# Kernel tuning notes

Measured on AMD Instinct MI355X. Metric: run time of the kernel, lower is better.

## Reference

```python
import jax, jax.numpy as jnp
import numpy as np

NEG = -1e30  # safe -inf surrogate for fp32 log-space DP
BLANK = 0


def setup_inputs() -> dict:
    key = jax.random.key(0)
    k1, k2 = jax.random.split(key)
    T, B, V, S = 2048, 64, 256, 256
    log_probs = jax.random.normal(k1, (T, B, V), dtype=jnp.float32)
    # targets exclude the blank index (0), as standard for CTC
    targets = jax.random.randint(k2, (B, S), 1, V).astype(jnp.int64)
    input_lengths = jnp.full((B,), T, dtype=jnp.int64)
    target_lengths = jnp.full((B,), S, dtype=jnp.int64)
    return {
        "log_probs": log_probs,
        "targets": targets,
        "input_lengths": input_lengths,
        "target_lengths": target_lengths,
    }


def _ctc_loss(log_probs, targets, input_lengths, target_lengths):
    """Numerically-stable CTC forward DP. log_probs: [T,B,V] (already log-softmaxed).
    Matches torch.nn.CTCLoss(blank=0, reduction='mean', zero_infinity=True)."""
    T, B, V = log_probs.shape
    S = targets.shape[1]
    L = 2 * S + 1  # extended label length (blanks interleaved)

    # extended label sequence: [blank, t0, blank, t1, ..., tS-1, blank]
    ext = jnp.full((B, L), BLANK, dtype=targets.dtype).at[:, 1::2].set(targets)

    # per-state emission log-probs: lp_ext[t, b, s] = log_probs[t, b, ext[b, s]]
    b_idx = jnp.arange(B)[:, None]
    lp_ext = log_probs[:, b_idx, ext]  # [T, B, L]

    # skip transition allowed when ext[s] != blank and ext[s] != ext[s-2]
    prev2 = jnp.pad(ext[:, :-2], ((0, 0), (2, 0)), constant_values=-1)
    skip = (ext != BLANK) & (ext != prev2)  # [B, L]

    alpha0 = jnp.full((B, L), NEG, dtype=log_probs.dtype)
    alpha0 = alpha0.at[:, 0].set(lp_ext[0, :, 0]).at[:, 1].set(lp_ext[0, :, 1])

    def step(alpha, xs):
        lp_t, t = xs
        a1 = jnp.pad(alpha[:, :-1], ((0, 0), (1, 0)), constant_values=NEG)
        a2 = jnp.pad(alpha[:, :-2], ((0, 0), (2, 0)), constant_values=NEG)
        comb = jnp.logaddexp(alpha, a1)
        comb = jnp.where(skip, jnp.logaddexp(comb, a2), comb)
        new = comb + lp_t
        # freeze alpha once past each sequence's input length
        new = jnp.where((t < input_lengths)[:, None], new, alpha)
        return new, None

    alpha, _ = jax.lax.scan(step, alpha0, (lp_ext[1:], jnp.arange(1, T)))

    end1 = jnp.take_along_axis(alpha, (2 * target_lengths)[:, None], axis=1)[:, 0]
    end2 = jnp.take_along_axis(alpha, (2 * target_lengths - 1)[:, None], axis=1)[:, 0]
    loss = -jnp.logaddexp(end1, end2)  # [B]

    # zero_infinity=True
    loss = jnp.where(jnp.isfinite(loss) & (loss < 1e29), loss, 0.0)
    # reduction='mean': divide each loss by its target length, then batch-mean
    return jnp.mean(loss / target_lengths.astype(loss.dtype))


def reference(log_probs, targets, input_lengths, target_lengths):
    # apply_log_softmax=True in the wrapper's forward
    log_probs = jax.nn.log_softmax(log_probs, axis=-1)
    return _ctc_loss(log_probs, targets, input_lengths, target_lengths)
```

## Files before the change

kernel.cpp:

```cpp
#include <hip/hip_runtime.h>
#include <hip/hip_fp16.h>
#include <stdint.h>

#define TT 2048
#define BB 64
#define VV 256
#define SS 256
#define LL 513

#define F_L2E 1.4426950408889634f
#define F_LN2 0.6931471805599453f
#define TGT_E 40
#define MARG  50
#define KOFF  262144

static __device__ __forceinline__ float exp2_fast(float x) {
  float r; asm("v_exp_f32 %0, %1" : "=v"(r) : "v"(x)); return r;
}
static __device__ __forceinline__ float log2_fast(float x) {
  float r; asm("v_log_f32 %0, %1" : "=v"(r) : "v"(x)); return r;
}
static __device__ __forceinline__ void g2l16(const void* g, void* l) {
  __builtin_amdgcn_global_load_lds((const __attribute__((address_space(1))) void*)g,
                                   (__attribute__((address_space(3))) void*)l, 16, 0, 0);
}
static __device__ __forceinline__ float dpp_shr1_f(float x) {
  int r = __builtin_amdgcn_update_dpp(0, __float_as_int(x), 0x138, 0xF, 0xF, true);
  return __int_as_float(r);
}
static __device__ __forceinline__ int dpp_shr1_i(int x) {
  return __builtin_amdgcn_update_dpp(0, x, 0x138, 0xF, 0xF, true);
}
template <int CTRL, int RMASK>
static __device__ __forceinline__ int dppmax_i(int v) {
  int d = __builtin_amdgcn_update_dpp(v, v, CTRL, RMASK, 0xF, false);
  return v > d ? v : d;
}
static __device__ __forceinline__ int scanmax_i(int v) {
  v = dppmax_i<0x111, 0xF>(v);
  v = dppmax_i<0x112, 0xF>(v);
  v = dppmax_i<0x114, 0xF>(v);
  v = dppmax_i<0x118, 0xF>(v);
  v = dppmax_i<0x142, 0xa>(v);
  v = dppmax_i<0x143, 0xc>(v);
  return v;
}

__global__ __launch_bounds__(256) void k_prep2(const float* __restrict__ lp,
                                               const int* __restrict__ tgt,
                                               __half* __restrict__ Eg,
                                               float* __restrict__ Bl,
                                               float* __restrict__ D2T) {
  __shared__ int tgtl[SS];
  __shared__ __half elds[4][VV];
  int b  = blockIdx.x & (BB - 1);
  int t0 = (blockIdx.x >> 6) << 2;
  int tid = threadIdx.x;
  tgtl[tid] = tgt[b * SS + tid];
  __syncthreads();
  int w = tid >> 6, lane = tid & 63;
  int t = t0 + w;
  float4 x = reinterpret_cast<const float4*>(lp + ((size_t)t * BB + b) * VV)[lane];
  float e0 = exp2_fast(x.x * F_L2E), e1 = exp2_fast(x.y * F_L2E);
  float e2 = exp2_fast(x.z * F_L2E), e3 = exp2_fast(x.w * F_L2E);
  float z = (e0 + e1) + (e2 + e3);
  z += __shfl_xor(z, 1);
  z += __shfl_xor(z, 2);
  z += __shfl_xor(z, 4);
  z += __shfl_xor(z, 8);
  z += __shfl_xor(z, 16);
  z += __shfl_xor(z, 32);
  elds[w][4 * lane + 0] = __float2half_rn(e0);
  elds[w][4 * lane + 1] = __float2half_rn(e1);
  elds[w][4 * lane + 2] = __float2half_rn(e2);
  elds[w][4 * lane + 3] = __float2half_rn(e3);
  asm volatile("s_waitcnt lgkmcnt(0)" ::: "memory");
  int s = 4 * lane;
  union { __half h[4]; uint2 u; } pk;
  pk.h[0] = elds[w][tgtl[s + 0]];
  pk.h[1] = elds[w][tgtl[s + 1]];
  pk.h[2] = elds[w][tgtl[s + 2]];
  pk.h[3] = elds[w][tgtl[s + 3]];
  reinterpret_cast<uint2*>(Eg + ((size_t)b * TT + t) * SS)[lane] = pk.u;
  if (lane == 0) {
    Bl[(size_t)b * TT + t]  = e0;
    D2T[(size_t)b * TT + t] = -log2_fast(z);
  }
}

__global__ __launch_bounds__(64) void k_ctc6(const __half* __restrict__ Eg,
                                             const float* __restrict__ Bl,
                                             const int* __restrict__ tgt,
                                             const int* __restrict__ ilen,
                                             const int* __restrict__ tlen,
                                             const float* __restrict__ D2T,
                                             float* __restrict__ lossw) {
  __shared__ float blanklds[TT];
  __shared__ float afin[LL];
  __shared__ int   cfinl[64];
  int b = blockIdx.x, lane = threadIdx.x;
  int len = ilen[b]; if (len > TT) len = TT; if (len < 0) len = 0;
  int tl  = tlen[b]; if (tl > SS) tl = SS; if (tl < 1) tl = 1;

  const float* blb = Bl  + (size_t)b * TT;
  const float* d2b = D2T + (size_t)b * TT;
  const uint2* eq  = reinterpret_cast<const uint2*>(Eg) + (size_t)b * TT * 64 + lane;

  int4 tv = reinterpret_cast<const int4*>(tgt + b * SS)[lane];
  int pw  = __shfl_up(tv.w, 1);
  float mk1 = (lane > 0 && tv.x != pw) ? 1.f : 0.f;
  float mk3 = (tv.y != tv.x) ? 1.f : 0.f;
  float mk5 = (tv.z != tv.y) ? 1.f : 0.f;
  float mk7 = (tv.w != tv.z) ? 1.f : 0.f;

#pragma unroll
  for (int j = 0; j < 8; ++j)
    g2l16(blb + j * 256 + lane * 4, &blanklds[j * 256]);

  uint2 pfA[16], pfB[16];
#pragma unroll
  for (int j = 0; j < 16; ++j) pfA[j] = eq[(size_t)j * 64];
  asm volatile("s_waitcnt vmcnt(0)" ::: "memory");

  float a0 = (lane == 0) ? 1.f : 0.f;
  float a1 = 0, a2 = 0, a3 = 0, a4 = 0, a5 = 0, a6 = 0, a7 = 0, a8 = 0;
  int C = 0;
  int diffi = 0;

#define STEP32(BANK, J, TB) do {                                               \
    uint2 pv = pf##BANK[J];                                                    \
    float2 flo = __half22float2(*reinterpret_cast<const __half2*>(&pv.x));     \
    float2 fhi = __half22float2(*reinterpret_cast<const __half2*>(&pv.y));     \
    float pb = blanklds[(TB) + (J)];                                           \
    float h1 = ldexpf(dpp_shr1_f(a7), diffi);                                  \
    a8 = (a8 + a7) * pb;                                                       \
    a7 = (a7 + a6 + mk7 * a5) * fhi.y;                                         \
    a6 = (a6 + a5) * pb;                                                       \
    a5 = (a5 + a4 + mk5 * a3) * fhi.x;                                         \
    a4 = (a4 + a3) * pb;                                                       \
    a3 = (a3 + a2 + mk3 * a1) * flo.y;                                         \
    a2 = (a2 + a1) * pb;                                                       \
    a1 = (a1 + a0 + mk1 * h1) * flo.x;                                         \
    a0 = (a0 + h1) * pb;                                                       \
  } while (0)

#define RESCALE8() do {                                                        \
    float mx = fmaxf(fmaxf(fmaxf(a0, a1), fmaxf(a2, a3)),                      \
                     fmaxf(fmaxf(a4, a5), fmaxf(fmaxf(a6, a7), a8)));          \
    bool live_ = (mx > 0.f);                                                   \
    int e_  = (int)((__float_as_uint(mx) >> 23) & 0xff);                       \
    int Cl_ = C + e_ - (127 + TGT_E);                                          \
    int key_ = live_ ? (Cl_ + KOFF) : 0;                                       \
    key_ = scanmax_i(key_);                                                    \
    int Cn_ = (key_ - KOFF) - MARG;                                            \
    if (live_ && Cl_ > Cn_) Cn_ = Cl_;                                         \
    int shE_ = Cn_ - C;                                                        \
    a0 = ldexpf(a0, -shE_); a1 = ldexpf(a1, -shE_); a2 = ldexpf(a2, -shE_);    \
    a3 = ldexpf(a3, -shE_); a4 = ldexpf(a4, -shE_); a5 = ldexpf(a5, -shE_);    \
    a6 = ldexpf(a6, -shE_); a7 = ldexpf(a7, -shE_); a8 = ldexpf(a8, -shE_);    \
    C = Cn_;                                                                   \
    diffi = dpp_shr1_i(C) - C;                                                 \
  } while (0)

#define ISSUE16(BANK, TBN) do {                                                \
    const uint2* p_ = eq + (size_t)(TBN) * 64;                                 \
    _Pragma("unroll")                                                          \
    for (int j_ = 0; j_ < 16; ++j_) pf##BANK[j_] = p_[(size_t)j_ * 64];        \
  } while (0)

#define BLK16(CUR, NXT, TB) do {                                               \
    int tbn_ = (TB) + 16; if (tbn_ > TT - 16) tbn_ = TT - 16;                  \
    ISSUE16(NXT, tbn_);                                                        \
    asm volatile("s_waitcnt vmcnt(16)" ::: "memory");                          \
    STEP32(CUR, 0, (TB));  STEP32(CUR, 1, (TB));  STEP32(CUR, 2, (TB));        \
    STEP32(CUR, 3, (TB));  STEP32(CUR, 4, (TB));  STEP32(CUR, 5, (TB));        \
    STEP32(CUR, 6, (TB));  STEP32(CUR, 7, (TB));                               \
    RESCALE8();                                                                \
    STEP32(CUR, 8, (TB));  STEP32(CUR, 9, (TB));  STEP32(CUR, 10, (TB));       \
    STEP32(CUR, 11, (TB)); STEP32(CUR, 12, (TB)); STEP32(CUR, 13, (TB));       \
    STEP32(CUR, 14, (TB)); STEP32(CUR, 15, (TB));                              \
    RESCALE8();                                                                \
  } while (0)

  int tcur = 0;
  for (int g = 0; g < TT / 32 && tcur + 32 <= len; ++g) {
    BLK16(A, B, tcur);
    BLK16(B, A, tcur + 16);
    tcur += 32;
  }

  if (tcur < len) {
    asm volatile("s_waitcnt vmcnt(0)" ::: "memory");
    while (tcur < len) {
      uint2 pv = eq[(size_t)tcur * 64];
      float2 flo = __half22float2(*reinterpret_cast<const __half2*>(&pv.x));
      float2 fhi = __half22float2(*reinterpret_cast<const __half2*>(&pv.y));
      float pb = blanklds[tcur];
      float h1 = ldexpf(dpp_shr1_f(a7), diffi);
      a8 = (a8 + a7) * pb;
      a7 = (a7 + a6 + mk7 * a5) * fhi.y;
      a6 = (a6 + a5) * pb;
      a5 = (a5 + a4 + mk5 * a3) * fhi.x;
      a4 = (a4 + a3) * pb;
      a3 = (a3 + a2 + mk3 * a1) * flo.y;
      a2 = (a2 + a1) * pb;
      a1 = (a1 + a0 + mk1 * h1) * flo.x;
      a0 = (a0 + h1) * pb;
      ++tcur;
      if ((tcur & 7) == 0) RESCALE8();
    }
  }

  float dsm = 0.f;
  for (int k2 = 0; k2 < TT / 64; ++k2) {
    int t2 = lane + 64 * k2;
    if (t2 < len) dsm += d2b[t2];
  }
  dsm += __shfl_xor(dsm, 1);
  dsm += __shfl_xor(dsm, 2);
  dsm += __shfl_xor(dsm, 4);
  dsm += __shfl_xor(dsm, 8);
  dsm += __shfl_xor(dsm, 16);
  dsm += __shfl_xor(dsm, 32);

  afin[8 * lane + 0] = a0; afin[8 * lane + 1] = a1;
  afin[8 * lane + 2] = a2; afin[8 * lane + 3] = a3;
  afin[8 * lane + 4] = a4; afin[8 * lane + 5] = a5;
  afin[8 * lane + 6] = a6; afin[8 * lane + 7] = a7;
  if (lane == 63) afin[512] = a8;
  cfinl[lane] = C;
  __syncthreads();
  if (lane == 0) {
    int s1 = 2 * tl, s2 = 2 * tl - 1;
    float v1 = afin[s1], v2 = afin[s2];
    int C1 = cfinl[s1 >= 512 ? 63 : (s1 >> 3)];
    int C2 = cfinl[s2 >= 512 ? 63 : (s2 >> 3)];
    float l1 = (v1 > 0.f) ? (log2_fast(v1) + (float)C1) : -1e30f;
    float l2 = (v2 > 0.f) ? (log2_fast(v2) + (float)C2) : -1e30f;
    float m  = fmaxf(l1, l2);
    float r  = m + log2_fast(exp2_fast(l1 - m) + exp2_fast(l2 - m));
    lossw[b] = -F_LN2 * (r + dsm);
  }
#undef STEP32
#undef RESCALE8
#undef ISSUE16
#undef BLK16
}

__global__ __launch_bounds__(64) void k_final(const float* __restrict__ lossw,
                                              const int* __restrict__ tlen,
                                              float* __restrict__ out) {
  int i = threadIdx.x;
  float v = lossw[i];
  float d = (float)tlen[i];
  v = (v < 1e29f && v > -1e30f) ? (v / d) : 0.f;
  v += __shfl_xor(v, 1);
  v += __shfl_xor(v, 2);
  v += __shfl_xor(v, 4);
  v += __shfl_xor(v, 8);
  v += __shfl_xor(v, 16);
  v += __shfl_xor(v, 32);
  if (i == 0) out[0] = v * (1.f / BB);
}

extern "C" void kernel_launch(void* const* d_in, const int* in_sizes, int n_in,
                              void* d_out, int out_size, void* d_ws, size_t ws_size,
                              hipStream_t stream) {
  const float* lp = (const float*)d_in[0];
  const int* tgt  = (const int*)d_in[1];
  const int* ilen = (const int*)d_in[2];
  const int* tlen = (const int*)d_in[3];

  size_t eg_bytes = (size_t)BB * TT * SS * 2;
  __half* Eg   = (__half*)d_ws;
  float* Bl    = (float*)((char*)d_ws + eg_bytes);
  float* D2T   = Bl + (size_t)BB * TT;
  float* lossw = D2T + (size_t)BB * TT;

  k_prep2<<<BB * (TT / 4), 256, 0, stream>>>(lp, tgt, Eg, Bl, D2T);
  k_ctc6<<<BB, 64, 0, stream>>>(Eg, Bl, tgt, ilen, tlen, D2T, lossw);
  k_final<<<1, 64, 0, stream>>>(lossw, tlen, (float*)d_out);
}
```

Before: 168.0 us.

## Triple-buffer emission prefetch and hoist blank-prob LDS reads in CTC recurrence

```diff
diff --git a/kernel.cpp b/kernel.cpp
--- a/kernel.cpp
+++ b/kernel.cpp
@@ -88,7 +88,7 @@
   }
 }
 
-__global__ __launch_bounds__(64) void k_ctc6(const __half* __restrict__ Eg,
+__global__ __launch_bounds__(64) void k_ctc7(const __half* __restrict__ Eg,
                                              const float* __restrict__ Bl,
                                              const int* __restrict__ tgt,
                                              const int* __restrict__ ilen,
@@ -117,21 +117,23 @@
   for (int j = 0; j < 8; ++j)
     g2l16(blb + j * 256 + lane * 4, &blanklds[j * 256]);
 
-  uint2 pfA[16], pfB[16];
-#pragma unroll
-  for (int j = 0; j < 16; ++j) pfA[j] = eq[(size_t)j * 64];
-  asm volatile("s_waitcnt vmcnt(0)" ::: "memory");
-
+  uint2 pfA[16], pfB[16], pfC[16];
   float a0 = (lane == 0) ? 1.f : 0.f;
   float a1 = 0, a2 = 0, a3 = 0, a4 = 0, a5 = 0, a6 = 0, a7 = 0, a8 = 0;
   int C = 0;
   int diffi = 0;
 
-#define STEP32(BANK, J, TB) do {                                               \
+#define ISSUE16(BANK, TBN) do {                                                \
+    const uint2* p_ = eq + (size_t)(TBN) * 64;                                 \
+    _Pragma("unroll")                                                          \
+    for (int j_ = 0; j_ < 16; ++j_) pf##BANK[j_] = p_[(size_t)j_ * 64];        \
+  } while (0)
+
+#define STEP32(BANK, J) do {                                                   \
     uint2 pv = pf##BANK[J];                                                    \
     float2 flo = __half22float2(*reinterpret_cast<const __half2*>(&pv.x));     \
     float2 fhi = __half22float2(*reinterpret_cast<const __half2*>(&pv.y));     \
-    float pb = blanklds[(TB) + (J)];                                           \
+    float pb = pbreg[J];                                                       \
     float h1 = ldexpf(dpp_shr1_f(a7), diffi);                                  \
     a8 = (a8 + a7) * pb;                                                       \
     a7 = (a7 + a6 + mk7 * a5) * fhi.y;                                         \
@@ -162,31 +164,33 @@
     diffi = dpp_shr1_i(C) - C;                                                 \
   } while (0)
 
-#define ISSUE16(BANK, TBN) do {                                                \
-    const uint2* p_ = eq + (size_t)(TBN) * 64;                                 \
+#define BLK(CUR, NXT, TB, VMC) do {                                            \
+    if ((VMC) == 32) ISSUE16(NXT, (TB) + 32);                                  \
+    float pbreg[16];                                                           \
     _Pragma("unroll")                                                          \
-    for (int j_ = 0; j_ < 16; ++j_) pf##BANK[j_] = p_[(size_t)j_ * 64];        \
-  } while (0)
-
-#define BLK16(CUR, NXT, TB) do {                                               \
-    int tbn_ = (TB) + 16; if (tbn_ > TT - 16) tbn_ = TT - 16;                  \
-    ISSUE16(NXT, tbn_);                                                        \
-    asm volatile("s_waitcnt vmcnt(16)" ::: "memory");                          \
-    STEP32(CUR, 0, (TB));  STEP32(CUR, 1, (TB));  STEP32(CUR, 2, (TB));        \
-    STEP32(CUR, 3, (TB));  STEP32(CUR, 4, (TB));  STEP32(CUR, 5, (TB));        \
-    STEP32(CUR, 6, (TB));  STEP32(CUR, 7, (TB));                               \
+    for (int j_ = 0; j_ < 16; ++j_) pbreg[j_] = blanklds[(TB) + j_];           \
+    asm volatile("s_waitcnt vmcnt(%0)" :: "i"(VMC) : "memory");                \
+    STEP32(CUR, 0);  STEP32(CUR, 1);  STEP32(CUR, 2);  STEP32(CUR, 3);         \
+    STEP32(CUR, 4);  STEP32(CUR, 5);  STEP32(CUR, 6);  STEP32(CUR, 7);         \
     RESCALE8();                                                                \
-    STEP32(CUR, 8, (TB));  STEP32(CUR, 9, (TB));  STEP32(CUR, 10, (TB));       \
-    STEP32(CUR, 11, (TB)); STEP32(CUR, 12, (TB)); STEP32(CUR, 13, (TB));       \
-    STEP32(CUR, 14, (TB)); STEP32(CUR, 15, (TB));                              \
+    STEP32(CUR, 8);  STEP32(CUR, 9);  STEP32(CUR, 10); STEP32(CUR, 11);        \
+    STEP32(CUR, 12); STEP32(CUR, 13); STEP32(CUR, 14); STEP32(CUR, 15);        \
     RESCALE8();                                                                \
   } while (0)
 
   int tcur = 0;
-  for (int g = 0; g < TT / 32 && tcur + 32 <= len; ++g) {
-    BLK16(A, B, tcur);
-    BLK16(B, A, tcur + 16);
-    tcur += 32;
+  if (len == TT) {
+    ISSUE16(A, 0);
+    ISSUE16(B, 16);
+    for (int g = 0; g < 42; ++g) {
+      BLK(A, C, tcur, 32);
+      BLK(B, A, tcur + 16, 32);
+      BLK(C, B, tcur + 32, 32);
+      tcur += 48;
+    }
+    BLK(A, C, tcur, 16);
+    BLK(B, C, tcur + 16, 0);
+    tcur = TT;
   }
 
   if (tcur < len) {
@@ -207,7 +211,23 @@
       a1 = (a1 + a0 + mk1 * h1) * flo.x;
       a0 = (a0 + h1) * pb;
       ++tcur;
-      if ((tcur & 7) == 0) RESCALE8();
+      if ((tcur & 7) == 0) {
+        float mx = fmaxf(fmaxf(fmaxf(a0, a1), fmaxf(a2, a3)),
+                         fmaxf(fmaxf(a4, a5), fmaxf(fmaxf(a6, a7), a8)));
+        bool live_ = (mx > 0.f);
+        int e_  = (int)((__float_as_uint(mx) >> 23) & 0xff);
+        int Cl_ = C + e_ - (127 + TGT_E);
+        int key_ = live_ ? (Cl_ + KOFF) : 0;
+        key_ = scanmax_i(key_);
+        int Cn_ = (key_ - KOFF) - MARG;
+        if (live_ && Cl_ > Cn_) Cn_ = Cl_;
+        int shE_ = Cn_ - C;
+        a0 = ldexpf(a0, -shE_); a1 = ldexpf(a1, -shE_); a2 = ldexpf(a2, -shE_);
+        a3 = ldexpf(a3, -shE_); a4 = ldexpf(a4, -shE_); a5 = ldexpf(a5, -shE_);
+        a6 = ldexpf(a6, -shE_); a7 = ldexpf(a7, -shE_); a8 = ldexpf(a8, -shE_);
+        C = Cn_;
+        diffi = dpp_shr1_i(C) - C;
+      }
     }
   }
 
@@ -244,7 +264,7 @@
 #undef STEP32
 #undef RESCALE8
 #undef ISSUE16
-#undef BLK16
+#undef BLK
 }
 
 __global__ __launch_bounds__(64) void k_final(const float* __restrict__ lossw,
@@ -278,6 +298,6 @@
   float* lossw = D2T + (size_t)BB * TT;
 
   k_prep2<<<BB * (TT / 4), 256, 0, stream>>>(lp, tgt, Eg, Bl, D2T);
-  k_ctc6<<<BB, 64, 0, stream>>>(Eg, Bl, tgt, ilen, tlen, D2T, lossw);
+  k_ctc7<<<BB, 64, 0, stream>>>(Eg, Bl, tgt, ilen, tlen, D2T, lossw);
   k_final<<<1, 64, 0, stream>>>(lossw, tlen, (float*)d_out);
 }
```

Result: no change. 165.3 us (-1.6%).

## Interleave two batch items per wavefront in CTC recurrence to hide latency

Applied to the files above, without the earlier changes.

```diff
diff --git a/kernel.cpp b/kernel.cpp
--- a/kernel.cpp
+++ b/kernel.cpp
@@ -44,6 +44,11 @@
   v = dppmax_i<0x142, 0xa>(v);
   v = dppmax_i<0x143, 0xc>(v);
   return v;
+}
+static __device__ __forceinline__ float pow2f(int d) {
+  int dc = d > 126 ? 126 : d;
+  float s = __int_as_float((dc + 127) << 23);
+  return (d < -126) ? 0.f : s;
 }
 
 __global__ __launch_bounds__(256) void k_prep2(const float* __restrict__ lp,
@@ -88,163 +93,219 @@
   }
 }
 
-__global__ __launch_bounds__(64) void k_ctc6(const __half* __restrict__ Eg,
-                                             const float* __restrict__ Bl,
-                                             const int* __restrict__ tgt,
-                                             const int* __restrict__ ilen,
-                                             const int* __restrict__ tlen,
-                                             const float* __restrict__ D2T,
-                                             float* __restrict__ lossw) {
-  __shared__ float blanklds[TT];
-  __shared__ float afin[LL];
-  __shared__ int   cfinl[64];
-  int b = blockIdx.x, lane = threadIdx.x;
-  int len = ilen[b]; if (len > TT) len = TT; if (len < 0) len = 0;
-  int tl  = tlen[b]; if (tl > SS) tl = SS; if (tl < 1) tl = 1;
-
-  const float* blb = Bl  + (size_t)b * TT;
-  const float* d2b = D2T + (size_t)b * TT;
-  const uint2* eq  = reinterpret_cast<const uint2*>(Eg) + (size_t)b * TT * 64 + lane;
-
-  int4 tv = reinterpret_cast<const int4*>(tgt + b * SS)[lane];
-  int pw  = __shfl_up(tv.w, 1);
-  float mk1 = (lane > 0 && tv.x != pw) ? 1.f : 0.f;
-  float mk3 = (tv.y != tv.x) ? 1.f : 0.f;
-  float mk5 = (tv.z != tv.y) ? 1.f : 0.f;
-  float mk7 = (tv.w != tv.z) ? 1.f : 0.f;
+__global__ __launch_bounds__(64) void k_ctc10(const __half* __restrict__ Eg,
+                                              const float* __restrict__ Bl,
+                                              const int* __restrict__ tgt,
+                                              const int* __restrict__ ilen,
+                                              const int* __restrict__ tlen,
+                                              const float* __restrict__ D2T,
+                                              float* __restrict__ lossw) {
+  __shared__ float blanklds[2][TT];
+  __shared__ float afin[2][LL];
+  __shared__ int   cfinl[2][64];
+  int bA = blockIdx.x * 2, bB = bA + 1;
+  int lane = threadIdx.x;
+  int lenA = ilen[bA]; if (lenA > TT) lenA = TT; if (lenA < 0) lenA = 0;
+  int lenB = ilen[bB]; if (lenB > TT) lenB = TT; if (lenB < 0) lenB = 0;
+  int tlA  = tlen[bA]; if (tlA > SS) tlA = SS; if (tlA < 1) tlA = 1;
+  int tlB  = tlen[bB]; if (tlB > SS) tlB = SS; if (tlB < 1) tlB = 1;
+
+  const uint2* eqA = reinterpret_cast<const uint2*>(Eg) + (size_t)bA * TT * 64 + lane;
+  const uint2* eqB = reinterpret_cast<const uint2*>(Eg) + (size_t)bB * TT * 64 + lane;
+
+  int4 tvA = reinterpret_cast<const int4*>(tgt + bA * SS)[lane];
+  int4 tvB = reinterpret_cast<const int4*>(tgt + bB * SS)[lane];
+  int pwA = __shfl_up(tvA.w, 1), pwB = __shfl_up(tvB.w, 1);
+  float mk1A = (lane > 0 && tvA.x != pwA) ? 1.f : 0.f;
+  float mk3A = (tvA.y != tvA.x) ? 1.f : 0.f;
+  float mk5A = (tvA.z != tvA.y) ? 1.f : 0.f;
+  float mk7A = (tvA.w != tvA.z) ? 1.f : 0.f;
+  float mk1B = (lane > 0 && tvB.x != pwB) ? 1.f : 0.f;
+  float mk3B = (tvB.y != tvB.x) ? 1.f : 0.f;
+  float mk5B = (tvB.z != tvB.y) ? 1.f : 0.f;
+  float mk7B = (tvB.w != tvB.z) ? 1.f : 0.f;
 
 #pragma unroll
-  for (int j = 0; j < 8; ++j)
-    g2l16(blb + j * 256 + lane * 4, &blanklds[j * 256]);
-
-  uint2 pfA[16], pfB[16];
-#pragma unroll
-  for (int j = 0; j < 16; ++j) pfA[j] = eq[(size_t)j * 64];
-  asm volatile("s_waitcnt vmcnt(0)" ::: "memory");
-
-  float a0 = (lane == 0) ? 1.f : 0.f;
-  float a1 = 0, a2 = 0, a3 = 0, a4 = 0, a5 = 0, a6 = 0, a7 = 0, a8 = 0;
-  int C = 0;
-  int diffi = 0;
-
-#define STEP32(BANK, J, TB) do {                                               \
-    uint2 pv = pf##BANK[J];                                                    \
+  for (int j = 0; j < 8; ++j) {
+    g2l16(Bl + (size_t)bA * TT + j * 256 + lane * 4, &blanklds[0][j * 256]);
+    g2l16(Bl + (size_t)bB * TT + j * 256 + lane * 4, &blanklds[1][j * 256]);
+  }
+
+  uint2 pA0[8], pA1[8], pA2[8], pB0[8], pB1[8], pB2[8];
+  float aA0 = (lane == 0) ? 1.f : 0.f;
+  float aA1 = 0, aA2 = 0, aA3 = 0, aA4 = 0, aA5 = 0, aA6 = 0, aA7 = 0, aA8 = 0;
+  float aB0 = (lane == 0) ? 1.f : 0.f;
+  float aB1 = 0, aB2 = 0, aB3 = 0, aB4 = 0, aB5 = 0, aB6 = 0, aB7 = 0, aB8 = 0;
+  int   CA = 0, CB = 0;
+  float sc1fA = 1.f, sc1fB = 1.f;
+
+#define ISSUE8(S, K, TBN) do {                                                 \
+    const uint2* p_ = eq##S + (size_t)(TBN) * 64;                              \
+    _Pragma("unroll")                                                          \
+    for (int j_ = 0; j_ < 8; ++j_) p##S##K[j_] = p_[(size_t)j_ * 64];          \
+  } while (0)
+
+#define STEP1(S, K, J) do {                                                    \
+    uint2 pv = p##S##K[J];                                                     \
     float2 flo = __half22float2(*reinterpret_cast<const __half2*>(&pv.x));     \
     float2 fhi = __half22float2(*reinterpret_cast<const __half2*>(&pv.y));     \
-    float pb = blanklds[(TB) + (J)];                                           \
-    float h1 = ldexpf(dpp_shr1_f(a7), diffi);                                  \
-    a8 = (a8 + a7) * pb;                                                       \
-    a7 = (a7 + a6 + mk7 * a5) * fhi.y;                                         \
-    a6 = (a6 + a5) * pb;                                                       \
-    a5 = (a5 + a4 + mk5 * a3) * fhi.x;                                         \
-    a4 = (a4 + a3) * pb;                                                       \
-    a3 = (a3 + a2 + mk3 * a1) * flo.y;                                         \
-    a2 = (a2 + a1) * pb;                                                       \
-    a1 = (a1 + a0 + mk1 * h1) * flo.x;                                         \
-    a0 = (a0 + h1) * pb;                                                       \
+    float pb = pb##S[J];                                                       \
+    float h1 = dpp_shr1_f(a##S##7) * sc1f##S;                                  \
+    a##S##8 = (a##S##8 + a##S##7) * pb;                                        \
+    a##S##7 = (a##S##7 + a##S##6 + mk7##S * a##S##5) * fhi.y;                  \
+    a##S##6 = (a##S##6 + a##S##5) * pb;                                        \
+    a##S##5 = (a##S##5 + a##S##4 + mk5##S * a##S##3) * fhi.x;                  \
+    a##S##4 = (a##S##4 + a##S##3) * pb;                                        \
+    a##S##3 = (a##S##3 + a##S##2 + mk3##S * a##S##1) * flo.y;                  \
+    a##S##2 = (a##S##2 + a##S##1) * pb;                                        \
+    a##S##1 = (a##S##1 + a##S##0 + mk1##S * h1) * flo.x;                       \
+    a##S##0 = (a##S##0 + h1) * pb;                                             \
   } while (0)
 
-#define RESCALE8() do {                                                        \
-    float mx = fmaxf(fmaxf(fmaxf(a0, a1), fmaxf(a2, a3)),                      \
-                     fmaxf(fmaxf(a4, a5), fmaxf(fmaxf(a6, a7), a8)));          \
+#define RESCALE1(S) do {                                                       \
+    float mx = fmaxf(fmaxf(fmaxf(a##S##0, a##S##1), fmaxf(a##S##2, a##S##3)),  \
+                     fmaxf(fmaxf(a##S##4, a##S##5),                            \
+                           fmaxf(fmaxf(a##S##6, a##S##7), a##S##8)));          \
     bool live_ = (mx > 0.f);                                                   \
     int e_  = (int)((__float_as_uint(mx) >> 23) & 0xff);                       \
-    int Cl_ = C + e_ - (127 + TGT_E);                                          \
+    int Cl_ = C##S + e_ - (127 + TGT_E);                                       \
     int key_ = live_ ? (Cl_ + KOFF) : 0;                                       \
     key_ = scanmax_i(key_);                                                    \
     int Cn_ = (key_ - KOFF) - MARG;                                            \
     if (live_ && Cl_ > Cn_) Cn_ = Cl_;                                         \
-    int shE_ = Cn_ - C;                                                        \
-    a0 = ldexpf(a0, -shE_); a1 = ldexpf(a1, -shE_); a2 = ldexpf(a2, -shE_);    \
-    a3 = ldexpf(a3, -shE_); a4 = ldexpf(a4, -shE_); a5 = ldexpf(a5, -shE_);    \
-    a6 = ldexpf(a6, -shE_); a7 = ldexpf(a7, -shE_); a8 = ldexpf(a8, -shE_);    \
-    C = Cn_;                                                                   \
-    diffi = dpp_shr1_i(C) - C;                                                 \
+    int shE_ = Cn_ - C##S;                                                     \
+    a##S##0 = ldexpf(a##S##0, -shE_); a##S##1 = ldexpf(a##S##1, -shE_);        \
+    a##S##2 = ldexpf(a##S##2, -shE_); a##S##3 = ldexpf(a##S##3, -shE_);        \
+    a##S##4 = ldexpf(a##S##4, -shE_); a##S##5 = ldexpf(a##S##5, -shE_);        \
+    a##S##6 = ldexpf(a##S##6, -shE_); a##S##7 = ldexpf(a##S##7, -shE_);        \
+    a##S##8 = ldexpf(a##S##8, -shE_);                                          \
+    C##S = Cn_;                                                                \
+    int diffi_ = dpp_shr1_i(C##S) - C##S;                                      \
+    sc1f##S = pow2f(diffi_);                                                   \
   } while (0)
 
-#define ISSUE16(BANK, TBN) do {                                                \
-    const uint2* p_ = eq + (size_t)(TBN) * 64;                                 \
+#define BLK(K, KN, TB, VMC) do {                                               \
+    if ((VMC) == 32) { ISSUE8(A, KN, (TB) + 16); ISSUE8(B, KN, (TB) + 16); }   \
+    float pbA[8], pbB[8];                                                      \
     _Pragma("unroll")                                                          \
-    for (int j_ = 0; j_ < 16; ++j_) pf##BANK[j_] = p_[(size_t)j_ * 64];        \
+    for (int j_ = 0; j_ < 8; ++j_) {                                           \
+      pbA[j_] = blanklds[0][(TB) + j_];                                        \
+      pbB[j_] = blanklds[1][(TB) + j_];                                        \
+    }                                                                          \
+    asm volatile("s_waitcnt vmcnt(%0)" :: "i"(VMC) : "memory");                \
+    STEP1(A, K, 0); STEP1(B, K, 0); STEP1(A, K, 1); STEP1(B, K, 1);            \
+    STEP1(A, K, 2); STEP1(B, K, 2); STEP1(A, K, 3); STEP1(B, K, 3);            \
+    STEP1(A, K, 4); STEP1(B, K, 4); STEP1(A, K, 5); STEP1(B, K, 5);            \
+    STEP1(A, K, 6); STEP1(B, K, 6); STEP1(A, K, 7); STEP1(B, K, 7);            \
+    RESCALE1(A); RESCALE1(B);                                                  \
   } while (0)
 
-#define BLK16(CUR, NXT, TB) do {                                               \
-    int tbn_ = (TB) + 16; if (tbn_ > TT - 16) tbn_ = TT - 16;                  \
-    ISSUE16(NXT, tbn_);                                                        \
-    asm volatile("s_waitcnt vmcnt(16)" ::: "memory");                          \
-    STEP32(CUR, 0, (TB));  STEP32(CUR, 1, (TB));  STEP32(CUR, 2, (TB));        \
-    STEP32(CUR, 3, (TB));  STEP32(CUR, 4, (TB));  STEP32(CUR, 5, (TB));        \
-    STEP32(CUR, 6, (TB));  STEP32(CUR, 7, (TB));                               \
-    RESCALE8();                                                                \
-    STEP32(CUR, 8, (TB));  STEP32(CUR, 9, (TB));  STEP32(CUR, 10, (TB));       \
-    STEP32(CUR, 11, (TB)); STEP32(CUR, 12, (TB)); STEP32(CUR, 13, (TB));       \
-    STEP32(CUR, 14, (TB)); STEP32(CUR, 15, (TB));                              \
-    RESCALE8();                                                                \
-  } while (0)
-
-  int tcur = 0;
-  for (int g = 0; g < TT / 32 && tcur + 32 <= len; ++g) {
-    BLK16(A, B, tcur);
-    BLK16(B, A, tcur + 16);
-    tcur += 32;
-  }
-
-  if (tcur < len) {
+  if (lenA == TT && lenB == TT) {
+    ISSUE8(A, 0, 0);  ISSUE8(B, 0, 0);
+    ISSUE8(A, 1, 8);  ISSUE8(B, 1, 8);
+    asm volatile("s_waitcnt vmcnt(32)" ::: "memory");
+    int t = 0;
+    for (int g = 0; g < 84; ++g) {
+      BLK(0, 2, t, 32);
+      BLK(1, 0, t + 8, 32);
+      BLK(2, 1, t + 16, 32);
+      t += 24;
+    }
+    BLK(0, 2, 2016, 32);
+    BLK(1, 0, 2024, 32);
+    BLK(2, 0, 2032, 16);
+    BLK(0, 0, 2040, 0);
+  } else {
     asm volatile("s_waitcnt vmcnt(0)" ::: "memory");
-    while (tcur < len) {
-      uint2 pv = eq[(size_t)tcur * 64];
-      float2 flo = __half22float2(*reinterpret_cast<const __half2*>(&pv.x));
-      float2 fhi = __half22float2(*reinterpret_cast<const __half2*>(&pv.y));
-      float pb = blanklds[tcur];
-      float h1 = ldexpf(dpp_shr1_f(a7), diffi);
-      a8 = (a8 + a7) * pb;
-      a7 = (a7 + a6 + mk7 * a5) * fhi.y;
-      a6 = (a6 + a5) * pb;
-      a5 = (a5 + a4 + mk5 * a3) * fhi.x;
-      a4 = (a4 + a3) * pb;
-      a3 = (a3 + a2 + mk3 * a1) * flo.y;
-      a2 = (a2 + a1) * pb;
-      a1 = (a1 + a0 + mk1 * h1) * flo.x;
-      a0 = (a0 + h1) * pb;
-      ++tcur;
-      if ((tcur & 7) == 0) RESCALE8();
+    int tmax = lenA > lenB ? lenA : lenB;
+    for (int t = 0; t < tmax; ++t) {
+      if (t < lenA) {
+        uint2 pv = eqA[(size_t)t * 64];
+        float2 flo = __half22float2(*reinterpret_cast<const __half2*>(&pv.x));
+        float2 fhi = __half22float2(*reinterpret_cast<const __half2*>(&pv.y));
+        float pb = blanklds[0][t];
+        float h1 = dpp_shr1_f(aA7) * sc1fA;
+        aA8 = (aA8 + aA7) * pb;
+        aA7 = (aA7 + aA6 + mk7A * aA5) * fhi.y;
+        aA6 = (aA6 + aA5) * pb;
+        aA5 = (aA5 + aA4 + mk5A * aA3) * fhi.x;
+        aA4 = (aA4 + aA3) * pb;
+        aA3 = (aA3 + aA2 + mk3A * aA1) * flo.y;
+        aA2 = (aA2 + aA1) * pb;
+        aA1 = (aA1 + aA0 + mk1A * h1) * flo.x;
+        aA0 = (aA0 + h1) * pb;
+      }
+      if (t < lenB) {
+        uint2 pv = eqB[(size_t)t * 64];
+        float2 flo = __half22float2(*reinterpret_cast<const __half2*>(&pv.x));
+        float2 fhi = __half22float2(*reinterpret_cast<const __half2*>(&pv.y));
+        float pb = blanklds[1][t];
+        float h1 = dpp_shr1_f(aB7) * sc1fB;
+        aB8 = (aB8 + aB7) * pb;
+        aB7 = (aB7 + aB6 + mk7B * aB5) * fhi.y;
+        aB6 = (aB6 + aB5) * pb;
+        aB5 = (aB5 + aB4 + mk5B * aB3) * fhi.x;
+        aB4 = (aB4 + aB3) * pb;
+        aB3 = (aB3 + aB2 + mk3B * aB1) * flo.y;
+        aB2 = (aB2 + aB1) * pb;
+        aB1 = (aB1 + aB0 + mk1B * h1) * flo.x;
+        aB0 = (aB0 + h1) * pb;
+      }
+      if (((t + 1) & 7) == 0) { RESCALE1(A); RESCALE1(B); }
     }
   }
 
-  float dsm = 0.f;
+  float dsmA = 0.f, dsmB = 0.f;
   for (int k2 = 0; k2 < TT / 64; ++k2) {
     int t2 = lane + 64 * k2;
-    if (t2 < len) dsm += d2b[t2];
-  }
-  dsm += __shfl_xor(dsm, 1);
-  dsm += __shfl_xor(dsm, 2);
-  dsm += __shfl_xor(dsm, 4);
-  dsm += __shfl_xor(dsm, 8);
-  dsm += __shfl_xor(dsm, 16);
-  dsm += __shfl_xor(dsm, 32);
-
-  afin[8 * lane + 0] = a0; afin[8 * lane + 1] = a1;
-  afin[8 * lane + 2] = a2; afin[8 * lane + 3] = a3;
-  afin[8 * lane + 4] = a4; afin[8 * lane + 5] = a5;
-  afin[8 * lane + 6] = a6; afin[8 * lane + 7] = a7;
-  if (lane == 63) afin[512] = a8;
-  cfinl[lane] = C;
+    if (t2 < lenA) dsmA += D2T[(size_t)bA * TT + t2];
+    if (t2 < lenB) dsmB += D2T[(size_t)bB * TT + t2];
+  }
+#pragma unroll
+  for (int sh = 1; sh < 64; sh <<= 1) {
+    dsmA += __shfl_xor(dsmA, sh);
+    dsmB += __shfl_xor(dsmB, sh);
+  }
+
+  afin[0][8 * lane + 0] = aA0; afin[0][8 * lane + 1] = aA1;
+  afin[0][8 * lane + 2] = aA2; afin[0][8 * lane + 3] = aA3;
+  afin[0][8 * lane + 4] = aA4; afin[0][8 * lane + 5] = aA5;
+  afin[0][8 * lane + 6] = aA6; afin[0][8 * lane + 7] = aA7;
+  afin[1][8 * lane + 0] = aB0; afin[1][8 * lane + 1] = aB1;
+  afin[1][8 * lane + 2] = aB2; afin[1][8 * lane + 3] = aB3;
+  afin[1][8 * lane + 4] = aB4; afin[1][8 * lane + 5] = aB5;
+  afin[1][8 * lane + 6] = aB6; afin[1][8 * lane + 7] = aB7;
+  if (lane == 63) { afin[0][512] = aA8; afin[1][512] = aB8; }
+  cfinl[0][lane] = CA; cfinl[1][lane] = CB;
   __syncthreads();
   if (lane == 0) {
-    int s1 = 2 * tl, s2 = 2 * tl - 1;
-    float v1 = afin[s1], v2 = afin[s2];
-    int C1 = cfinl[s1 >= 512 ? 63 : (s1 >> 3)];
-    int C2 = cfinl[s2 >= 512 ? 63 : (s2 >> 3)];
-    float l1 = (v1 > 0.f) ? (log2_fast(v1) + (float)C1) : -1e30f;
-    float l2 = (v2 > 0.f) ? (log2_fast(v2) + (float)C2) : -1e30f;
-    float m  = fmaxf(l1, l2);
-    float r  = m + log2_fast(exp2_fast(l1 - m) + exp2_fast(l2 - m));
-    lossw[b] = -F_LN2 * (r + dsm);
-  }
-#undef STEP32
-#undef RESCALE8
-#undef ISSUE16
-#undef BLK16
+    {
+      int s1 = 2 * tlA, s2 = 2 * tlA - 1;
+      float v1 = afin[0][s1], v2 = afin[0][s2];
+      int C1 = cfinl[0][s1 >= 512 ? 63 : (s1 >> 3)];
+      int C2 = cfinl[0][s2 >= 512 ? 63 : (s2 >> 3)];
+      float l1 = (v1 > 0.f) ? (log2_fast(v1) + (float)C1) : -1e30f;
+      float l2 = (v2 > 0.f) ? (log2_fast(v2) + (float)C2) : -1e30f;
+      float m  = fmaxf(l1, l2);
+      float r  = m + log2_fast(exp2_fast(l1 - m) + exp2_fast(l2 - m));
+      lossw[bA] = -F_LN2 * (r + dsmA);
+    }
+    {
+      int s1 = 2 * tlB, s2 = 2 * tlB - 1;
+      float v1 = afin[1][s1], v2 = afin[1][s2];
+      int C1 = cfinl[1][s1 >= 512 ? 63 : (s1 >> 3)];
+      int C2 = cfinl[1][s2 >= 512 ? 63 : (s2 >> 3)];
+      float l1 = (v1 > 0.f) ? (log2_fast(v1) + (float)C1) : -1e30f;
+      float l2 = (v2 > 0.f) ? (log2_fast(v2) + (float)C2) : -1e30f;
+      float m  = fmaxf(l1, l2);
+      float r  = m + log2_fast(exp2_fast(l1 - m) + exp2_fast(l2 - m));
+      lossw[bB] = -F_LN2 * (r + dsmB);
+    }
+  }
+#undef ISSUE8
+#undef STEP1
+#undef RESCALE1
+#undef BLK
 }
 
 __global__ __launch_bounds__(64) void k_final(const float* __restrict__ lossw,
@@ -278,6 +339,6 @@
   float* lossw = D2T + (size_t)BB * TT;
 
   k_prep2<<<BB * (TT / 4), 256, 0, stream>>>(lp, tgt, Eg, Bl, D2T);
-  k_ctc6<<<BB, 64, 0, stream>>>(Eg, Bl, tgt, ilen, tlen, D2T, lossw);
+  k_ctc10<<<BB / 2, 64, 0, stream>>>(Eg, Bl, tgt, ilen, tlen, D2T, lossw);
   k_final<<<1, 64, 0, stream>>>(lossw, tlen, (float*)d_out);
 }
```

Result: slower. 292.5 us (+74.1%).

## Split CTC state chain across two wavefronts with wavefront-pipelined time chunks

Applied to the files above, without the earlier changes.

```diff
diff --git a/kernel.cpp b/kernel.cpp
--- a/kernel.cpp
+++ b/kernel.cpp
@@ -7,6 +7,8 @@
 #define VV 256
 #define SS 256
 #define LL 513
+#define CH 8
+#define NCH (TT / CH)
 
 #define F_L2E 1.4426950408889634f
 #define F_LN2 0.6931471805599453f
@@ -44,6 +46,11 @@
   v = dppmax_i<0x142, 0xa>(v);
   v = dppmax_i<0x143, 0xc>(v);
   return v;
+}
+static __device__ __forceinline__ float pow2f(int d) {
+  int dc = d > 126 ? 126 : d;
+  float s = __int_as_float((dc + 127) << 23);
+  return (d < -126) ? 0.f : s;
 }
 
 __global__ __launch_bounds__(256) void k_prep2(const float* __restrict__ lp,
@@ -88,163 +95,215 @@
   }
 }
 
-__global__ __launch_bounds__(64) void k_ctc6(const __half* __restrict__ Eg,
-                                             const float* __restrict__ Bl,
-                                             const int* __restrict__ tgt,
-                                             const int* __restrict__ ilen,
-                                             const int* __restrict__ tlen,
-                                             const float* __restrict__ D2T,
-                                             float* __restrict__ lossw) {
+__global__ __launch_bounds__(128) void k_ctc11(const __half* __restrict__ Eg,
+                                               const float* __restrict__ Bl,
+                                               const int* __restrict__ tgt,
+                                               const int* __restrict__ ilen,
+                                               const int* __restrict__ tlen,
+                                               const float* __restrict__ D2T,
+                                               float* __restrict__ lossw) {
   __shared__ float blanklds[TT];
+  __shared__ float bring[4][CH];
+  __shared__ int   bringC[4][2];
+  __shared__ float bzero[CH];
+  __shared__ int   bzeroC[2];
   __shared__ float afin[LL];
-  __shared__ int   cfinl[64];
-  int b = blockIdx.x, lane = threadIdx.x;
+  __shared__ int   cfinl[128];
+
+  int tid = threadIdx.x;
+  int wid = tid >> 6, lane = tid & 63;
+  int b = blockIdx.x;
   int len = ilen[b]; if (len > TT) len = TT; if (len < 0) len = 0;
   int tl  = tlen[b]; if (tl > SS) tl = SS; if (tl < 1) tl = 1;
 
-  const float* blb = Bl  + (size_t)b * TT;
-  const float* d2b = D2T + (size_t)b * TT;
-  const uint2* eq  = reinterpret_cast<const uint2*>(Eg) + (size_t)b * TT * 64 + lane;
-
-  int4 tv = reinterpret_cast<const int4*>(tgt + b * SS)[lane];
-  int pw  = __shfl_up(tv.w, 1);
-  float mk1 = (lane > 0 && tv.x != pw) ? 1.f : 0.f;
+  if (tid < CH) bzero[tid] = 0.f;
+  if (tid < 2)  bzeroC[tid] = 0;
+
+  if (wid == 0) {
+#pragma unroll
+    for (int j = 0; j < 8; ++j)
+      g2l16(Bl + (size_t)b * TT + j * 256 + lane * 4, &blanklds[j * 256]);
+  }
+
+  int s0 = wid * 128 + 2 * lane;
+  int2 tv = reinterpret_cast<const int2*>(tgt + b * SS)[wid * 64 + lane];
+  int pv = __shfl_up(tv.y, 1);
+  if (lane == 0) pv = (s0 > 0) ? tgt[b * SS + s0 - 1] : 0;
+  float mk1 = (s0 > 0 && tv.x != pv) ? 1.f : 0.f;
   float mk3 = (tv.y != tv.x) ? 1.f : 0.f;
-  float mk5 = (tv.z != tv.y) ? 1.f : 0.f;
-  float mk7 = (tv.w != tv.z) ? 1.f : 0.f;
+
+  const unsigned* equ = reinterpret_cast<const unsigned*>(Eg)
+                      + (size_t)b * TT * 128 + wid * 64 + lane;
+
+  float b0 = (tid == 0) ? 1.f : 0.f, b1 = 0.f, b2 = 0.f, b3 = 0.f, btp = 0.f;
+  int   C = 0;
+  float sc1f = 1.f;
+  unsigned gA[CH], gB[CH];
+  float rb[CH];
 
 #pragma unroll
-  for (int j = 0; j < 8; ++j)
-    g2l16(blb + j * 256 + lane * 4, &blanklds[j * 256]);
-
-  uint2 pfA[16], pfB[16];
-#pragma unroll
-  for (int j = 0; j < 16; ++j) pfA[j] = eq[(size_t)j * 64];
-  asm volatile("s_waitcnt vmcnt(0)" ::: "memory");
-
-  float a0 = (lane == 0) ? 1.f : 0.f;
-  float a1 = 0, a2 = 0, a3 = 0, a4 = 0, a5 = 0, a6 = 0, a7 = 0, a8 = 0;
-  int C = 0;
-  int diffi = 0;
-
-#define STEP32(BANK, J, TB) do {                                               \
-    uint2 pv = pf##BANK[J];                                                    \
-    float2 flo = __half22float2(*reinterpret_cast<const __half2*>(&pv.x));     \
-    float2 fhi = __half22float2(*reinterpret_cast<const __half2*>(&pv.y));     \
-    float pb = blanklds[(TB) + (J)];                                           \
-    float h1 = ldexpf(dpp_shr1_f(a7), diffi);                                  \
-    a8 = (a8 + a7) * pb;                                                       \
-    a7 = (a7 + a6 + mk7 * a5) * fhi.y;                                         \
-    a6 = (a6 + a5) * pb;                                                       \
-    a5 = (a5 + a4 + mk5 * a3) * fhi.x;                                         \
-    a4 = (a4 + a3) * pb;                                                       \
-    a3 = (a3 + a2 + mk3 * a1) * flo.y;                                         \
-    a2 = (a2 + a1) * pb;                                                       \
-    a1 = (a1 + a0 + mk1 * h1) * flo.x;                                         \
-    a0 = (a0 + h1) * pb;                                                       \
+  for (int j = 0; j < CH; ++j) gA[j] = equ[(size_t)j * 128];
+
+  asm volatile("s_waitcnt lgkmcnt(0)" ::: "memory");
+  __builtin_amdgcn_s_barrier();
+
+#define STEPW(BK, J) do {                                                      \
+    rb[J] = b3;                                                                \
+    unsigned pv_ = g##BK[J];                                                   \
+    float2 fq = __half22float2(*reinterpret_cast<const __half2*>(&pv_));       \
+    float pb = pbg[J];                                                         \
+    float h1d = dpp_shr1_f(b3) * sc1f;                                         \
+    float h1 = (lane == 0) ? hb[J] : h1d;                                      \
+    btp = (btp + b3) * pb;                                                     \
+    b3 = (b3 + b2 + mk3 * b1) * fq.y;                                          \
+    b2 = (b2 + b1) * pb;                                                       \
+    b1 = (b1 + b0 + mk1 * h1) * fq.x;                                          \
+    b0 = (b0 + h1) * pb;                                                       \
   } while (0)
 
-#define RESCALE8() do {                                                        \
-    float mx = fmaxf(fmaxf(fmaxf(a0, a1), fmaxf(a2, a3)),                      \
-                     fmaxf(fmaxf(a4, a5), fmaxf(fmaxf(a6, a7), a8)));          \
+#define RESCW(BSEED) do {                                                      \
+    float mx = fmaxf(fmaxf(fmaxf(b0, b1), fmaxf(b2, b3)), btp);                \
     bool live_ = (mx > 0.f);                                                   \
-    int e_  = (int)((__float_as_uint(mx) >> 23) & 0xff);                       \
+    int e_ = (int)((__float_as_uint(mx) >> 23) & 0xff);                        \
     int Cl_ = C + e_ - (127 + TGT_E);                                          \
     int key_ = live_ ? (Cl_ + KOFF) : 0;                                       \
+    int sd_ = (lane == 0) ? (BSEED) : 0;                                       \
+    key_ = key_ > sd_ ? key_ : sd_;                                            \
     key_ = scanmax_i(key_);                                                    \
     int Cn_ = (key_ - KOFF) - MARG;                                            \
     if (live_ && Cl_ > Cn_) Cn_ = Cl_;                                         \
     int shE_ = Cn_ - C;                                                        \
-    a0 = ldexpf(a0, -shE_); a1 = ldexpf(a1, -shE_); a2 = ldexpf(a2, -shE_);    \
-    a3 = ldexpf(a3, -shE_); a4 = ldexpf(a4, -shE_); a5 = ldexpf(a5, -shE_);    \
-    a6 = ldexpf(a6, -shE_); a7 = ldexpf(a7, -shE_); a8 = ldexpf(a8, -shE_);    \
+    b0 = ldexpf(b0, -shE_); b1 = ldexpf(b1, -shE_);                            \
+    b2 = ldexpf(b2, -shE_); b3 = ldexpf(b3, -shE_);                            \
+    btp = ldexpf(btp, -shE_);                                                  \
     C = Cn_;                                                                   \
-    diffi = dpp_shr1_i(C) - C;                                                 \
+    int diffi_ = dpp_shr1_i(C) - C;                                            \
+    sc1f = pow2f(diffi_);                                                      \
   } while (0)
 
-#define ISSUE16(BANK, TBN) do {                                                \
-    const uint2* p_ = eq + (size_t)(TBN) * 64;                                 \
+#define PROC(BKC, BKN, c_) do {                                                \
+    int tb_ = (c_) * CH;                                                       \
+    int tn_ = tb_ + CH; if (tn_ > TT - CH) tn_ = TT - CH;                      \
     _Pragma("unroll")                                                          \
-    for (int j_ = 0; j_ < 16; ++j_) pf##BANK[j_] = p_[(size_t)j_ * 64];        \
+    for (int j_ = 0; j_ < CH; ++j_) g##BKN[j_] = equ[(size_t)(tn_ + j_) * 128];\
+    int sl_ = (c_) & 3;                                                        \
+    const float* bv_ = wid ? &bring[sl_][0] : bzero;                           \
+    const int*   bc_ = wid ? &bringC[sl_][0] : bzeroC;                         \
+    int craw_ = bc_[0]; int bseed_ = bc_[1];                                   \
+    int d_ = craw_ - C;                                                        \
+    float hb[CH];                                                              \
+    _Pragma("unroll")                                                          \
+    for (int j_ = 0; j_ < CH; ++j_) hb[j_] = ldexpf(bv_[j_], d_);              \
+    float pbg[CH];                                                             \
+    _Pragma("unroll")                                                          \
+    for (int j_ = 0; j_ < CH; ++j_) pbg[j_] = blanklds[tb_ + j_];              \
+    int Cpre_ = C;                                                             \
+    asm volatile("s_waitcnt vmcnt(8)" ::: "memory");                           \
+    STEPW(BKC, 0); STEPW(BKC, 1); STEPW(BKC, 2); STEPW(BKC, 3);                \
+    STEPW(BKC, 4); STEPW(BKC, 5); STEPW(BKC, 6); STEPW(BKC, 7);                \
+    RESCW(bseed_);                                                             \
+    if (wid == 0 && lane == 63) {                                              \
+      int ps_ = (c_) & 3;                                                      \
+      _Pragma("unroll")                                                        \
+      for (int j_ = 0; j_ < CH; ++j_) bring[ps_][j_] = rb[j_];                 \
+      bringC[ps_][0] = Cpre_;                                                  \
+      bringC[ps_][1] = C + KOFF;                                               \
+    }                                                                          \
   } while (0)
 
-#define BLK16(CUR, NXT, TB) do {                                               \
-    int tbn_ = (TB) + 16; if (tbn_ > TT - 16) tbn_ = TT - 16;                  \
-    ISSUE16(NXT, tbn_);                                                        \
-    asm volatile("s_waitcnt vmcnt(16)" ::: "memory");                          \
-    STEP32(CUR, 0, (TB));  STEP32(CUR, 1, (TB));  STEP32(CUR, 2, (TB));        \
-    STEP32(CUR, 3, (TB));  STEP32(CUR, 4, (TB));  STEP32(CUR, 5, (TB));        \
-    STEP32(CUR, 6, (TB));  STEP32(CUR, 7, (TB));                               \
-    RESCALE8();                                                                \
-    STEP32(CUR, 8, (TB));  STEP32(CUR, 9, (TB));  STEP32(CUR, 10, (TB));       \
-    STEP32(CUR, 11, (TB)); STEP32(CUR, 12, (TB)); STEP32(CUR, 13, (TB));       \
-    STEP32(CUR, 14, (TB)); STEP32(CUR, 15, (TB));                              \
-    RESCALE8();                                                                \
-  } while (0)
-
-  int tcur = 0;
-  for (int g = 0; g < TT / 32 && tcur + 32 <= len; ++g) {
-    BLK16(A, B, tcur);
-    BLK16(B, A, tcur + 16);
-    tcur += 32;
-  }
-
-  if (tcur < len) {
+  if (len == TT) {
+#pragma unroll 1
+    for (int k = 0; k < NCH + 2; k += 2) {
+      {
+        int c = k - 2 * wid;
+        if (c >= 0 && c < NCH) PROC(A, B, c);
+        asm volatile("s_waitcnt lgkmcnt(0)" ::: "memory");
+        __builtin_amdgcn_s_barrier();
+      }
+      {
+        int c = k + 1 - 2 * wid;
+        if (c >= 0 && c < NCH) PROC(B, A, c);
+        asm volatile("s_waitcnt lgkmcnt(0)" ::: "memory");
+        __builtin_amdgcn_s_barrier();
+      }
+    }
+  } else {
     asm volatile("s_waitcnt vmcnt(0)" ::: "memory");
-    while (tcur < len) {
-      uint2 pv = eq[(size_t)tcur * 64];
-      float2 flo = __half22float2(*reinterpret_cast<const __half2*>(&pv.x));
-      float2 fhi = __half22float2(*reinterpret_cast<const __half2*>(&pv.y));
-      float pb = blanklds[tcur];
-      float h1 = ldexpf(dpp_shr1_f(a7), diffi);
-      a8 = (a8 + a7) * pb;
-      a7 = (a7 + a6 + mk7 * a5) * fhi.y;
-      a6 = (a6 + a5) * pb;
-      a5 = (a5 + a4 + mk5 * a3) * fhi.x;
-      a4 = (a4 + a3) * pb;
-      a3 = (a3 + a2 + mk3 * a1) * flo.y;
-      a2 = (a2 + a1) * pb;
-      a1 = (a1 + a0 + mk1 * h1) * flo.x;
-      a0 = (a0 + h1) * pb;
-      ++tcur;
-      if ((tcur & 7) == 0) RESCALE8();
+    int nit = (len + CH - 1) / CH + 2;
+    for (int k = 0; k < nit; ++k) {
+      int c = k - 2 * wid;
+      int tb = c * CH;
+      if (c >= 0 && tb < len) {
+        int sl = c & 3;
+        const float* bv_ = wid ? &bring[sl][0] : bzero;
+        const int*   bc_ = wid ? &bringC[sl][0] : bzeroC;
+        int craw_ = bc_[0], bseed_ = bc_[1];
+        int d_ = craw_ - C;
+        int Cpre_ = C;
+        float rbs[CH];
+        for (int j = 0; j < CH; ++j) {
+          int t = tb + j;
+          rbs[j] = b3;
+          if (t < len) {
+            unsigned pv_ = equ[(size_t)t * 128];
+            float2 fq = __half22float2(*reinterpret_cast<const __half2*>(&pv_));
+            float pb = blanklds[t];
+            float h1d = dpp_shr1_f(b3) * sc1f;
+            float h1 = (lane == 0) ? ldexpf(bv_[j], d_) : h1d;
+            btp = (btp + b3) * pb;
+            b3 = (b3 + b2 + mk3 * b1) * fq.y;
+            b2 = (b2 + b1) * pb;
+            b1 = (b1 + b0 + mk1 * h1) * fq.x;
+            b0 = (b0 + h1) * pb;
+          }
+        }
+        RESCW(bseed_);
+        if (wid == 0 && lane == 63) {
+          int ps = c & 3;
+          for (int j = 0; j < CH; ++j) bring[ps][j] = rbs[j];
+          bringC[ps][0] = Cpre_;
+          bringC[ps][1] = C + KOFF;
+        }
+      }
+      asm volatile("s_waitcnt lgkmcnt(0)" ::: "memory");
+      __builtin_amdgcn_s_barrier();
     }
   }
 
   float dsm = 0.f;
-  for (int k2 = 0; k2 < TT / 64; ++k2) {
-    int t2 = lane + 64 * k2;
-    if (t2 < len) dsm += d2b[t2];
-  }
-  dsm += __shfl_xor(dsm, 1);
-  dsm += __shfl_xor(dsm, 2);
-  dsm += __shfl_xor(dsm, 4);
-  dsm += __shfl_xor(dsm, 8);
-  dsm += __shfl_xor(dsm, 16);
-  dsm += __shfl_xor(dsm, 32);
-
-  afin[8 * lane + 0] = a0; afin[8 * lane + 1] = a1;
-  afin[8 * lane + 2] = a2; afin[8 * lane + 3] = a3;
-  afin[8 * lane + 4] = a4; afin[8 * lane + 5] = a5;
-  afin[8 * lane + 6] = a6; afin[8 * lane + 7] = a7;
-  if (lane == 63) afin[512] = a8;
-  cfinl[lane] = C;
+  if (wid == 0) {
+    for (int k2 = 0; k2 < TT / 64; ++k2) {
+      int t2 = lane + 64 * k2;
+      if (t2 < len) dsm += D2T[(size_t)b * TT + t2];
+    }
+    dsm += __shfl_xor(dsm, 1);
+    dsm += __shfl_xor(dsm, 2);
+    dsm += __shfl_xor(dsm, 4);
+    dsm += __shfl_xor(dsm, 8);
+    dsm += __shfl_xor(dsm, 16);
+    dsm += __shfl_xor(dsm, 32);
+  }
+
+  int glane = wid * 64 + lane;
+  afin[4 * glane + 0] = b0; afin[4 * glane + 1] = b1;
+  afin[4 * glane + 2] = b2; afin[4 * glane + 3] = b3;
+  if (tid == 127) afin[512] = btp;
+  cfinl[glane] = C;
   __syncthreads();
-  if (lane == 0) {
+  if (tid == 0) {
     int s1 = 2 * tl, s2 = 2 * tl - 1;
     float v1 = afin[s1], v2 = afin[s2];
-    int C1 = cfinl[s1 >= 512 ? 63 : (s1 >> 3)];
-    int C2 = cfinl[s2 >= 512 ? 63 : (s2 >> 3)];
+    int C1 = cfinl[s1 >= 512 ? 127 : (s1 >> 2)];
+    int C2 = cfinl[s2 >= 512 ? 127 : (s2 >> 2)];
     float l1 = (v1 > 0.f) ? (log2_fast(v1) + (float)C1) : -1e30f;
     float l2 = (v2 > 0.f) ? (log2_fast(v2) + (float)C2) : -1e30f;
     float m  = fmaxf(l1, l2);
     float r  = m + log2_fast(exp2_fast(l1 - m) + exp2_fast(l2 - m));
     lossw[b] = -F_LN2 * (r + dsm);
   }
-#undef STEP32
-#undef RESCALE8
-#undef ISSUE16
-#undef BLK16
+#undef STEPW
+#undef RESCW
+#undef PROC
 }
 
 __global__ __launch_bounds__(64) void k_final(const float* __restrict__ lossw,
@@ -278,6 +337,6 @@
   float* lossw = D2T + (size_t)BB * TT;
 
   k_prep2<<<BB * (TT / 4), 256, 0, stream>>>(lp, tgt, Eg, Bl, D2T);
-  k_ctc6<<<BB, 64, 0, stream>>>(Eg, Bl, tgt, ilen, tlen, D2T, lossw);
+  k_ctc11<<<BB, 128, 0, stream>>>(Eg, Bl, tgt, ilen, tlen, D2T, lossw);
   k_final<<<1, 64, 0, stream>>>(lossw, tlen, (float*)d_out);
 }
```

New measurement: 220.0 us. 31.0% more time.
